# Performance work log

Hardware: AMD Instinct MI355X
Metric: run time of the kernel (lower is better)

Reference implementation:

```python
import jax, jax.numpy as jnp
import numpy as np

N, C, D, H, W = 1, 32, 64, 192, 160


def affine_grid_3d(theta, size):
    # PyTorch F.affine_grid 3D, align_corners=True convention.
    n, c, d, h, w = size
    z = jnp.linspace(-1.0, 1.0, d)
    y = jnp.linspace(-1.0, 1.0, h)
    x = jnp.linspace(-1.0, 1.0, w)
    zz, yy, xx = jnp.meshgrid(z, y, x, indexing='ij')          # [D,H,W]
    base = jnp.stack([xx, yy, zz, jnp.ones_like(xx)], axis=-1)  # [D,H,W,4]
    return jnp.einsum('dhwk,nck->ndhwc', base, theta)           # [N,D,H,W,3] (x,y,z)


def _gather_corner(vol, zi, yi, xi):
    # vol: [C,D,H,W]; zi/yi/xi: [D,H,W] int32. Zero padding outside.
    c, d, h, w = vol.shape
    valid = (zi >= 0) & (zi < d) & (yi >= 0) & (yi < h) & (xi >= 0) & (xi < w)
    zc = jnp.clip(zi, 0, d - 1)
    yc = jnp.clip(yi, 0, h - 1)
    xc = jnp.clip(xi, 0, w - 1)
    flat = vol.reshape(c, d * h * w)
    idx = (zc * h + yc) * w + xc
    vals = jnp.take(flat, idx.reshape(-1), axis=1).reshape(c, *zi.shape)
    return vals * valid[None].astype(vol.dtype)


def grid_sample_3d(inp, grid):
    # Trilinear grid_sample, zeros padding, align_corners=True.
    n, c, d, h, w = inp.shape
    x = (grid[..., 0] + 1.0) * 0.5 * (w - 1)
    y = (grid[..., 1] + 1.0) * 0.5 * (h - 1)
    z = (grid[..., 2] + 1.0) * 0.5 * (d - 1)
    x0 = jnp.floor(x).astype(jnp.int32); x1 = x0 + 1
    y0 = jnp.floor(y).astype(jnp.int32); y1 = y0 + 1
    z0 = jnp.floor(z).astype(jnp.int32); z1 = z0 + 1
    wx = (x - x0.astype(x.dtype))
    wy = (y - y0.astype(y.dtype))
    wz = (z - z0.astype(z.dtype))

    def sample_one(vol, z0, z1, y0, y1, x0, x1, wz, wy, wx):
        out = jnp.zeros((vol.shape[0],) + wz.shape, dtype=vol.dtype)
        for zi, wzc in ((z0, 1.0 - wz), (z1, wz)):
            for yi, wyc in ((y0, 1.0 - wy), (y1, wy)):
                for xi, wxc in ((x0, 1.0 - wx), (x1, wx)):
                    out = out + _gather_corner(vol, zi, yi, xi) * (wzc * wyc * wxc)[None]
        return out

    return jax.vmap(sample_one)(inp, z0, z1, y0, y1, x0, x1, wz, wy, wx)


def setup_inputs() -> dict:
    key = jax.random.key(0)
    k1, k2 = jax.random.split(key)
    inp = jax.random.normal(k1, (N, C, D, H, W), dtype=jnp.float32)
    identity = jnp.asarray([1, 0, 0, 0, 0, 1, 0, 0, 0, 0, 1, 0], dtype=jnp.float32)
    theta = identity + 0.1 * jax.random.normal(k2, (12,), dtype=jnp.float32)
    return {"input": inp, "theta": theta}


def reference(input, theta):
    th = theta.reshape(1, 3, 4)
    grid = affine_grid_3d(th, input.shape)       # [N,D,H,W,3]
    out = grid_sample_3d(input, grid)            # [N,C,D,H,W]
    return jnp.transpose(out, (0, 4, 3, 1, 2))   # [N,W,H,C,D]
```

## Files before the change

### kernel.cpp

```cpp
#include <hip/hip_runtime.h>

constexpr int W_ = 160;
constexpr int H_ = 192;
constexpr int D_ = 64;
constexpr int C_ = 32;
constexpr int HW_  = H_ * W_;
constexpr int DHWi = D_ * HW_;
constexpr int CD   = C_ * D_;

constexpr int TW = 32, TH = 12, TD = 16;
constexpr int NWT = W_ / TW;
constexpr int NHT = H_ / TH;
constexpr int NDT = D_ / TD;
constexpr int QPP = NWT * NHT;
constexpr int CPX = C_ / 8;
constexpr int NPH = CPX * NDT;
constexpr int LDS_BYTES = 36864;

typedef float f4_t __attribute__((ext_vector_type(4)));
typedef float f2_t __attribute__((ext_vector_type(2)));

__global__ void __launch_bounds__(256, 4)
affine_grid_sample_kernel(const float* __restrict__ inp,
                          const float* __restrict__ th,
                          float* __restrict__ out)
{
    extern __shared__ float smem[];

    const int t   = threadIdx.x;
    const int bid = blockIdx.x;
    const int xcd = bid & 7;
    int r = bid >> 3;
    const int phase = r / QPP;
    const int q     = r - phase * QPP;
    const int c  = xcd * CPX + (phase >> 2);
    const int dt = phase & 3;
    const int hs = q / NWT;
    const int wt = q - hs * NWT;
    const int w0 = wt * TW, h0 = hs * TH, d0 = dt * TD;

    if (bid < 0) smem[t] = 0.0f;

    const float th0=th[0], th1=th[1], th2 =th[2],  th3 =th[3];
    const float th4=th[4], th5=th[5], th6 =th[6],  th7 =th[7];
    const float th8=th[8], th9=th[9], th10=th[10], th11=th[11];

    const float* __restrict__ pc = inp + (size_t)c * DHWi;

    const int wl = t & 15;
    const int dq = (t >> 4) & 3;
    const int wh = (t >> 6) & 1;
    const int hp = t >> 7;
    const int w  = w0 + wh * 16 + wl;
    const float xx = fmaf((float)w, 2.0f / (W_ - 1), -1.0f);

    float kzx[4], kzy[4], kzz[4];
    #pragma unroll
    for (int k = 0; k < 4; ++k) {
        const int d = d0 + 4 * dq + k;
        const float zz = fmaf((float)d, 2.0f / (D_ - 1), -1.0f);
        kzx[k] = fmaf(th2,  zz, th3);
        kzy[k] = fmaf(th6,  zz, th7);
        kzz[k] = fmaf(th10, zz, th11);
    }

    float* const ob = out + ((size_t)w * H_ + h0) * CD + (size_t)c * D_ + d0 + 4 * dq;

    #pragma unroll 1
    for (int hh = hp; hh < TH; hh += 2) {
        const float yy = fmaf((float)(h0 + hh), 2.0f / (H_ - 1), -1.0f);

        unsigned off[4][4];
        float wA[4], wB[4], v0a[4], v1a[4], s0a[4], s1a[4];
        #pragma unroll
        for (int k = 0; k < 4; ++k) {
            const float px = (fmaf(th0, xx, fmaf(th1, yy, kzx[k])) + 1.0f) * (0.5f * (W_ - 1));
            const float py = (fmaf(th4, xx, fmaf(th5, yy, kzy[k])) + 1.0f) * (0.5f * (H_ - 1));
            const float pz = (fmaf(th8, xx, fmaf(th9, yy, kzz[k])) + 1.0f) * (0.5f * (D_ - 1));
            const float fx = floorf(px), fy = floorf(py), fz = floorf(pz);
            const int ix0 = (int)fx, iy0 = (int)fy, iz0 = (int)fz;
            const float wx = px - fx, wy = py - fy, wz = pz - fz;
            const float u0r = ((unsigned)ix0       < (unsigned)W_) ? (1.0f - wx) : 0.0f;
            const float u1r = ((unsigned)(ix0 + 1) < (unsigned)W_) ? wx          : 0.0f;
            v0a[k] = ((unsigned)iy0       < (unsigned)H_) ? (1.0f - wy) : 0.0f;
            v1a[k] = ((unsigned)(iy0 + 1) < (unsigned)H_) ? wy          : 0.0f;
            s0a[k] = ((unsigned)iz0       < (unsigned)D_) ? (1.0f - wz) : 0.0f;
            s1a[k] = ((unsigned)(iz0 + 1) < (unsigned)D_) ? wz          : 0.0f;
            float a = u0r, b = u1r;
            if (ix0 == -1)     { a = u1r; b = 0.0f; }
            if (ix0 == W_ - 1) { a = 0.0f; b = u0r; }
            wA[k] = a; wB[k] = b;
            const int e = min(max(ix0, 0), W_ - 2);
            const int cy0 = min(max(iy0,     0), H_ - 1);
            const int cy1 = min(max(iy0 + 1, 0), H_ - 1);
            const int cz0 = min(max(iz0,     0), D_ - 1);
            const int cz1 = min(max(iz0 + 1, 0), D_ - 1);
            off[k][0] = (unsigned)(cz0 * HW_ + cy0 * W_ + e);
            off[k][1] = (unsigned)(cz0 * HW_ + cy1 * W_ + e);
            off[k][2] = (unsigned)(cz1 * HW_ + cy0 * W_ + e);
            off[k][3] = (unsigned)(cz1 * HW_ + cy1 * W_ + e);
        }

        f2_t P[4][4];
        #pragma unroll
        for (int k = 0; k < 4; ++k)
            #pragma unroll
            for (int j = 0; j < 4; ++j)
                __builtin_memcpy(&P[k][j], pc + off[k][j], 8);

        asm volatile("" ::
            "v"(P[0][0]), "v"(P[0][1]), "v"(P[0][2]), "v"(P[0][3]),
            "v"(P[1][0]), "v"(P[1][1]), "v"(P[1][2]), "v"(P[1][3]),
            "v"(P[2][0]), "v"(P[2][1]), "v"(P[2][2]), "v"(P[2][3]),
            "v"(P[3][0]), "v"(P[3][1]), "v"(P[3][2]), "v"(P[3][3]));
        __builtin_amdgcn_sched_barrier(0);

        f4_t val;
        #pragma unroll
        for (int k = 0; k < 4; ++k) {
            const float x00 = wA[k] * P[k][0][0] + wB[k] * P[k][0][1];
            const float x01 = wA[k] * P[k][1][0] + wB[k] * P[k][1][1];
            const float x10 = wA[k] * P[k][2][0] + wB[k] * P[k][2][1];
            const float x11 = wA[k] * P[k][3][0] + wB[k] * P[k][3][1];
            const float e0 = v0a[k] * x00 + v1a[k] * x01;
            const float e1 = v0a[k] * x10 + v1a[k] * x11;
            val[k] = s0a[k] * e0 + s1a[k] * e1;
        }
        __builtin_nontemporal_store(val, (f4_t*)(ob + (size_t)hh * CD));
    }
}

extern "C" void kernel_launch(void* const* d_in, const int* in_sizes, int n_in,
                              void* d_out, int out_size, void* d_ws, size_t ws_size,
                              hipStream_t stream)
{
    const float* inp = (const float*)d_in[0];
    const float* th  = (const float*)d_in[1];
    float* out = (float*)d_out;

    hipLaunchKernelGGL(affine_grid_sample_kernel, dim3(8 * NPH * QPP), dim3(256),
                       LDS_BYTES, stream, inp, th, out);
}
```

Baseline: 633.0 us.

## Double-buffer gather loads across h iterations with software pipelining

Restructures the per-row loop into a fully unrolled two-stage software pipeline: the next row's coordinates are computed and its 16 gathers issued before the current row's loads are consumed. This hides global gather latency behind the previous iteration's arithmetic. It roughly doubles the live registers for gathered data and weights, which under launch_bounds(256,4) risks spills or lower occupancy.

```diff
diff --git a/kernel.cpp b/kernel.cpp
--- a/kernel.cpp
+++ b/kernel.cpp
@@ -19,6 +19,12 @@
 
 typedef float f4_t __attribute__((ext_vector_type(4)));
 typedef float f2_t __attribute__((ext_vector_type(2)));
+
+struct Stage {
+    unsigned off[4][4];
+    float wA[4], wB[4], v0[4], v1[4], s0[4], s1[4];
+    f2_t P[4][4];
+};
 
 __global__ void __launch_bounds__(256, 4)
 affine_grid_sample_kernel(const float* __restrict__ inp,
@@ -66,12 +72,8 @@
 
     float* const ob = out + ((size_t)w * H_ + h0) * CD + (size_t)c * D_ + d0 + 4 * dq;
 
-    #pragma unroll 1
-    for (int hh = hp; hh < TH; hh += 2) {
+    auto compute_stage = [&](Stage& S, int hh) {
         const float yy = fmaf((float)(h0 + hh), 2.0f / (H_ - 1), -1.0f);
-
-        unsigned off[4][4];
-        float wA[4], wB[4], v0a[4], v1a[4], s0a[4], s1a[4];
         #pragma unroll
         for (int k = 0; k < 4; ++k) {
             const float px = (fmaf(th0, xx, fmaf(th1, yy, kzx[k])) + 1.0f) * (0.5f * (W_ - 1));
@@ -82,51 +84,71 @@
             const float wx = px - fx, wy = py - fy, wz = pz - fz;
             const float u0r = ((unsigned)ix0       < (unsigned)W_) ? (1.0f - wx) : 0.0f;
             const float u1r = ((unsigned)(ix0 + 1) < (unsigned)W_) ? wx          : 0.0f;
-            v0a[k] = ((unsigned)iy0       < (unsigned)H_) ? (1.0f - wy) : 0.0f;
-            v1a[k] = ((unsigned)(iy0 + 1) < (unsigned)H_) ? wy          : 0.0f;
-            s0a[k] = ((unsigned)iz0       < (unsigned)D_) ? (1.0f - wz) : 0.0f;
-            s1a[k] = ((unsigned)(iz0 + 1) < (unsigned)D_) ? wz          : 0.0f;
+            S.v0[k] = ((unsigned)iy0       < (unsigned)H_) ? (1.0f - wy) : 0.0f;
+            S.v1[k] = ((unsigned)(iy0 + 1) < (unsigned)H_) ? wy          : 0.0f;
+            S.s0[k] = ((unsigned)iz0       < (unsigned)D_) ? (1.0f - wz) : 0.0f;
+            S.s1[k] = ((unsigned)(iz0 + 1) < (unsigned)D_) ? wz          : 0.0f;
             float a = u0r, b = u1r;
             if (ix0 == -1)     { a = u1r; b = 0.0f; }
             if (ix0 == W_ - 1) { a = 0.0f; b = u0r; }
-            wA[k] = a; wB[k] = b;
+            S.wA[k] = a; S.wB[k] = b;
             const int e = min(max(ix0, 0), W_ - 2);
             const int cy0 = min(max(iy0,     0), H_ - 1);
             const int cy1 = min(max(iy0 + 1, 0), H_ - 1);
             const int cz0 = min(max(iz0,     0), D_ - 1);
             const int cz1 = min(max(iz0 + 1, 0), D_ - 1);
-            off[k][0] = (unsigned)(cz0 * HW_ + cy0 * W_ + e);
-            off[k][1] = (unsigned)(cz0 * HW_ + cy1 * W_ + e);
-            off[k][2] = (unsigned)(cz1 * HW_ + cy0 * W_ + e);
-            off[k][3] = (unsigned)(cz1 * HW_ + cy1 * W_ + e);
+            S.off[k][0] = (unsigned)(cz0 * HW_ + cy0 * W_ + e);
+            S.off[k][1] = (unsigned)(cz0 * HW_ + cy1 * W_ + e);
+            S.off[k][2] = (unsigned)(cz1 * HW_ + cy0 * W_ + e);
+            S.off[k][3] = (unsigned)(cz1 * HW_ + cy1 * W_ + e);
         }
+    };
 
-        f2_t P[4][4];
+    auto issue_stage = [&](Stage& S) {
         #pragma unroll
         for (int k = 0; k < 4; ++k)
             #pragma unroll
             for (int j = 0; j < 4; ++j)
-                __builtin_memcpy(&P[k][j], pc + off[k][j], 8);
+                __builtin_memcpy(&S.P[k][j], pc + S.off[k][j], 8);
+    };
 
+    auto pin_stage = [&](Stage& S) {
         asm volatile("" ::
-            "v"(P[0][0]), "v"(P[0][1]), "v"(P[0][2]), "v"(P[0][3]),
-            "v"(P[1][0]), "v"(P[1][1]), "v"(P[1][2]), "v"(P[1][3]),
-            "v"(P[2][0]), "v"(P[2][1]), "v"(P[2][2]), "v"(P[2][3]),
-            "v"(P[3][0]), "v"(P[3][1]), "v"(P[3][2]), "v"(P[3][3]));
+            "v"(S.P[0][0]), "v"(S.P[0][1]), "v"(S.P[0][2]), "v"(S.P[0][3]),
+            "v"(S.P[1][0]), "v"(S.P[1][1]), "v"(S.P[1][2]), "v"(S.P[1][3]),
+            "v"(S.P[2][0]), "v"(S.P[2][1]), "v"(S.P[2][2]), "v"(S.P[2][3]),
+            "v"(S.P[3][0]), "v"(S.P[3][1]), "v"(S.P[3][2]), "v"(S.P[3][3]));
         __builtin_amdgcn_sched_barrier(0);
+    };
 
+    auto consume_stage = [&](Stage& S, int hh) {
         f4_t val;
         #pragma unroll
         for (int k = 0; k < 4; ++k) {
-            const float x00 = wA[k] * P[k][0][0] + wB[k] * P[k][0][1];
-            const float x01 = wA[k] * P[k][1][0] + wB[k] * P[k][1][1];
-            const float x10 = wA[k] * P[k][2][0] + wB[k] * P[k][2][1];
-            const float x11 = wA[k] * P[k][3][0] + wB[k] * P[k][3][1];
-            const float e0 = v0a[k] * x00 + v1a[k] * x01;
-            const float e1 = v0a[k] * x10 + v1a[k] * x11;
-            val[k] = s0a[k] * e0 + s1a[k] * e1;
+            const float x00 = S.wA[k] * S.P[k][0][0] + S.wB[k] * S.P[k][0][1];
+            const float x01 = S.wA[k] * S.P[k][1][0] + S.wB[k] * S.P[k][1][1];
+            const float x10 = S.wA[k] * S.P[k][2][0] + S.wB[k] * S.P[k][2][1];
+            const float x11 = S.wA[k] * S.P[k][3][0] + S.wB[k] * S.P[k][3][1];
+            const float e0 = S.v0[k] * x00 + S.v1[k] * x01;
+            const float e1 = S.v0[k] * x10 + S.v1[k] * x11;
+            val[k] = S.s0[k] * e0 + S.s1[k] * e1;
         }
         __builtin_nontemporal_store(val, (f4_t*)(ob + (size_t)hh * CD));
+    };
+
+    Stage SA, SB;
+    compute_stage(SA, hp);
+    issue_stage(SA);
+    #pragma unroll
+    for (int j = 0; j < 6; ++j) {
+        Stage& cur = (j & 1) ? SB : SA;
+        Stage& nxt = (j & 1) ? SA : SB;
+        if (j < 5) {
+            compute_stage(nxt, hp + 2 * (j + 1));
+            issue_stage(nxt);
+        }
+        pin_stage(cur);
+        consume_stage(cur, hp + 2 * j);
     }
 }
 
```

Result: slower. 744.0 us (+17.5%).

## Software-pipeline gathers with double-buffered registers across h iterations

Applied to the files above, without the earlier changes.

Splits each row iteration into an issue phase (compute offsets, launch the 16 gathers) and a consume phase (weights, interpolation, store). The loop is fully unrolled with two register buffers so the next row's loads are in flight while the current row is computed. This hides global-load latency but doubles the live gather registers and recomputes coordinates in both phases, which may cut occupancy under launch_bounds(256,4).

```diff
diff --git a/kernel.cpp b/kernel.cpp
--- a/kernel.cpp
+++ b/kernel.cpp
@@ -66,11 +66,35 @@
 
     float* const ob = out + ((size_t)w * H_ + h0) * CD + (size_t)c * D_ + d0 + 4 * dq;
 
-    #pragma unroll 1
-    for (int hh = hp; hh < TH; hh += 2) {
+    auto issue = [&](f2_t (&P)[4][4], int hh) {
         const float yy = fmaf((float)(h0 + hh), 2.0f / (H_ - 1), -1.0f);
+        #pragma unroll
+        for (int k = 0; k < 4; ++k) {
+            const float px = (fmaf(th0, xx, fmaf(th1, yy, kzx[k])) + 1.0f) * (0.5f * (W_ - 1));
+            const float py = (fmaf(th4, xx, fmaf(th5, yy, kzy[k])) + 1.0f) * (0.5f * (H_ - 1));
+            const float pz = (fmaf(th8, xx, fmaf(th9, yy, kzz[k])) + 1.0f) * (0.5f * (D_ - 1));
+            const int ix0 = (int)floorf(px);
+            const int iy0 = (int)floorf(py);
+            const int iz0 = (int)floorf(pz);
+            const int e   = min(max(ix0,     0), W_ - 2);
+            const int cy0 = min(max(iy0,     0), H_ - 1);
+            const int cy1 = min(max(iy0 + 1, 0), H_ - 1);
+            const int cz0 = min(max(iz0,     0), D_ - 1);
+            const int cz1 = min(max(iz0 + 1, 0), D_ - 1);
+            const unsigned o0 = (unsigned)(cz0 * HW_ + cy0 * W_ + e);
+            const unsigned o1 = (unsigned)(cz0 * HW_ + cy1 * W_ + e);
+            const unsigned o2 = (unsigned)(cz1 * HW_ + cy0 * W_ + e);
+            const unsigned o3 = (unsigned)(cz1 * HW_ + cy1 * W_ + e);
+            __builtin_memcpy(&P[k][0], pc + o0, 8);
+            __builtin_memcpy(&P[k][1], pc + o1, 8);
+            __builtin_memcpy(&P[k][2], pc + o2, 8);
+            __builtin_memcpy(&P[k][3], pc + o3, 8);
+        }
+        __builtin_amdgcn_sched_barrier(0);
+    };
 
-        unsigned off[4][4];
+    auto consume = [&](f2_t (&P)[4][4], int hh) {
+        const float yy = fmaf((float)(h0 + hh), 2.0f / (H_ - 1), -1.0f);
         float wA[4], wB[4], v0a[4], v1a[4], s0a[4], s1a[4];
         #pragma unroll
         for (int k = 0; k < 4; ++k) {
@@ -90,24 +114,7 @@
             if (ix0 == -1)     { a = u1r; b = 0.0f; }
             if (ix0 == W_ - 1) { a = 0.0f; b = u0r; }
             wA[k] = a; wB[k] = b;
-            const int e = min(max(ix0, 0), W_ - 2);
-            const int cy0 = min(max(iy0,     0), H_ - 1);
-            const int cy1 = min(max(iy0 + 1, 0), H_ - 1);
-            const int cz0 = min(max(iz0,     0), D_ - 1);
-            const int cz1 = min(max(iz0 + 1, 0), D_ - 1);
-            off[k][0] = (unsigned)(cz0 * HW_ + cy0 * W_ + e);
-            off[k][1] = (unsigned)(cz0 * HW_ + cy1 * W_ + e);
-            off[k][2] = (unsigned)(cz1 * HW_ + cy0 * W_ + e);
-            off[k][3] = (unsigned)(cz1 * HW_ + cy1 * W_ + e);
         }
-
-        f2_t P[4][4];
-        #pragma unroll
-        for (int k = 0; k < 4; ++k)
-            #pragma unroll
-            for (int j = 0; j < 4; ++j)
-                __builtin_memcpy(&P[k][j], pc + off[k][j], 8);
-
         asm volatile("" ::
             "v"(P[0][0]), "v"(P[0][1]), "v"(P[0][2]), "v"(P[0][3]),
             "v"(P[1][0]), "v"(P[1][1]), "v"(P[1][2]), "v"(P[1][3]),
@@ -127,6 +134,18 @@
             val[k] = s0a[k] * e0 + s1a[k] * e1;
         }
         __builtin_nontemporal_store(val, (f4_t*)(ob + (size_t)hh * CD));
+    };
+
+    f2_t PA[4][4], PB[4][4];
+    issue(PA, hp);
+    #pragma unroll
+    for (int j = 0; j < 6; ++j) {
+        if (j < 5) {
+            if (j & 1) issue(PA, hp + 2 * (j + 1));
+            else       issue(PB, hp + 2 * (j + 1));
+        }
+        if (j & 1) consume(PB, hp + 2 * j);
+        else       consume(PA, hp + 2 * j);
     }
 }
 
```

Result: no change. 637.8 us (+0.8%).
